# Optimization experiments

Measured on AMD Instinct MI355X. Metric: run time of the kernel, lower is better.

The kernel has to match this reference:

```python
import jax, jax.numpy as jnp
import numpy as np

B, L, D_MODEL = 4, 1024, 512
D_STATE, EXPAND, D_CONV = 16, 2, 4
D_INNER = EXPAND * D_MODEL
DT_RANK = D_MODEL // 16
NUM_LAYERS = 2
NL2 = 2 * NUM_LAYERS  # at/vt layer pairs, index 2*i -> at_i, 2*i+1 -> vt_i


def setup_inputs() -> dict:
    key = jax.random.key(0)
    ks = jax.random.split(key, 16)
    s = 0.02
    inp = {
        'a_x': jax.random.normal(ks[0], (B, L, D_MODEL), jnp.float32),
        'v_x': jax.random.normal(ks[1], (B, L, D_MODEL), jnp.float32),
        't_x': jax.random.normal(ks[2], (B, L, D_MODEL), jnp.float32),
        'in_proj_w': s * jax.random.normal(ks[3], (NL2, 2 * D_INNER, D_MODEL), jnp.float32),
        'conv_w': s * jax.random.normal(ks[4], (NL2, 2, D_INNER, D_CONV), jnp.float32),
        'conv_b': jnp.zeros((NL2, 2, D_INNER), jnp.float32),
        'xproj_w': s * jax.random.normal(ks[5], (NL2, 2, DT_RANK + 2 * D_STATE, D_INNER), jnp.float32),
        'dtproj_w': s * jax.random.normal(ks[6], (NL2, 2, D_INNER, DT_RANK), jnp.float32),
        'dtproj_b': 0.1 * jax.random.normal(ks[7], (NL2, 2, D_INNER), jnp.float32),
        'A_log': jnp.log(jnp.broadcast_to(jnp.arange(1.0, D_STATE + 1.0, dtype=jnp.float32), (NL2, 2, D_INNER, D_STATE))),
        'Dskip': jnp.ones((NL2, 2, D_INNER), jnp.float32),
        'out_proj_w': s * jax.random.normal(ks[8], (NL2, D_MODEL, D_INNER), jnp.float32),
        'ln_w': jnp.ones((NL2, 2, D_MODEL), jnp.float32),
        'ln_b': jnp.zeros((NL2, 2, D_MODEL), jnp.float32),
    }
    return inp


def layer_norm(x, w, b, eps=1e-6):
    m = jnp.mean(x, -1, keepdims=True)
    v = jnp.var(x, -1, keepdims=True)
    return (x - m) * jax.lax.rsqrt(v + eps) * w + b


def causal_conv1d(x, w, b):
    # x: (B,L,d), depthwise causal conv with kernel w: (d,k), bias b: (d,)
    y = jax.lax.conv_general_dilated(
        x.transpose(0, 2, 1), w[:, None, :], (1,), [(D_CONV - 1, 0)],
        feature_group_count=D_INNER,
        dimension_numbers=('NCH', 'OIH', 'NCH'))
    return y.transpose(0, 2, 1) + b


def selective_scan(u, dt, A, Bm, Cm, Dskip):
    # u,dt:(B,L,d)  A:(d,N)  Bm,Cm:(B,L,N)  Dskip:(d,)
    dA = jnp.exp(dt[..., None] * A)                    # (B,L,d,N)
    dBu = (dt * u)[..., None] * Bm[:, :, None, :]      # (B,L,d,N)

    def step(h, inp):
        dA_t, dBu_t, C_t = inp
        h = dA_t * h + dBu_t                           # (B,d,N)
        return h, jnp.einsum('bdn,bn->bd', h, C_t)

    h0 = jnp.zeros((u.shape[0], u.shape[2], D_STATE), u.dtype)
    xs = (jnp.moveaxis(dA, 1, 0), jnp.moveaxis(dBu, 1, 0), jnp.moveaxis(Cm, 1, 0))
    _, ys = jax.lax.scan(step, h0, xs)
    return jnp.moveaxis(ys, 0, 1) + u * Dskip


def _one_dir(x, cw, cb, xpw, dpw, dpb, A_log, Dskip):
    xc = jax.nn.silu(causal_conv1d(x, cw, cb))
    proj = xc @ xpw.T                                  # (B,L,dt_rank+2N)
    dt_r, Bm, Cm = jnp.split(proj, [DT_RANK, DT_RANK + D_STATE], axis=-1)
    dt = jax.nn.softplus(dt_r @ dpw.T + dpb)
    A = -jnp.exp(A_log)
    return selective_scan(xc, dt, A, Bm, Cm, Dskip)


def _bimamba(u, i, p):
    xz = u @ p['in_proj_w'][i].T
    x, z = jnp.split(xz, 2, axis=-1)
    yf = _one_dir(x, p['conv_w'][i, 0], p['conv_b'][i, 0], p['xproj_w'][i, 0],
                  p['dtproj_w'][i, 0], p['dtproj_b'][i, 0], p['A_log'][i, 0], p['Dskip'][i, 0])
    yb = _one_dir(x[:, ::-1], p['conv_w'][i, 1], p['conv_b'][i, 1], p['xproj_w'][i, 1],
                  p['dtproj_w'][i, 1], p['dtproj_b'][i, 1], p['A_log'][i, 1], p['Dskip'][i, 1])[:, ::-1]
    y = (yf + yb) * jax.nn.silu(z)
    return y @ p['out_proj_w'][i].T


def _enc_layer(a, t, i, p):
    ao = _bimamba(a, i, p)
    to = _bimamba(t, i, p)
    a_out = a + layer_norm(ao, p['ln_w'][i, 0], p['ln_b'][i, 0])
    t_out = t + layer_norm(to, p['ln_w'][i, 1], p['ln_b'][i, 1])
    return a_out, t_out


def reference(a_x, v_x, t_x, in_proj_w, conv_w, conv_b, xproj_w, dtproj_w, dtproj_b,
              A_log, Dskip, out_proj_w, ln_w, ln_b):
    p = dict(in_proj_w=in_proj_w, conv_w=conv_w, conv_b=conv_b, xproj_w=xproj_w,
             dtproj_w=dtproj_w, dtproj_b=dtproj_b, A_log=A_log, Dskip=Dskip,
             out_proj_w=out_proj_w, ln_w=ln_w, ln_b=ln_b)
    a_out, v_out, t_out = a_x, v_x, t_x
    for i in range(NUM_LAYERS):
        a_out, t_at = _enc_layer(a_out, t_out, 2 * i, p)
        v_out, t_vt = _enc_layer(v_out, t_out, 2 * i + 1, p)
        t_out = (t_at + t_vt) / 2
    return (a_out, v_out, t_out)
```

## Files before the change

### kernel.cpp

```cpp
#include <hip/hip_runtime.h>
#include <cstddef>

constexpr int B_      = 4;
constexpr int L_      = 1024;
constexpr int DM      = 512;
constexpr int DS      = 16;
constexpr int DI      = 1024;
constexpr int DTR     = 32;
constexpr int TOK     = B_ * L_;
constexpr int NLAYERS = 2;

constexpr size_t XZB = 0;
constexpr size_t XCB = (size_t)4 * TOK * 2 * DI * 2;
constexpr size_t PRB = XCB + (size_t)8 * TOK * DI * 2;
constexpr size_t WIB = PRB + (size_t)8 * TOK * 64 * 4;
constexpr size_t WOB = WIB + (size_t)4 * 2 * DI * DM * 2;
constexpr size_t WXB = WOB + (size_t)4 * DM * DI * 2;
constexpr size_t WS_NEED_BF = WXB + (size_t)8 * 64 * DI * 2;
constexpr size_t DTB2 = WS_NEED_BF;
constexpr size_t WS_NEED_DT = DTB2 + (size_t)8 * TOK * DI * 2;

constexpr int NCH = 16;
constexpr size_t PP_BYTE = (size_t)8 * 4 * NCH * 1024 * DS * 2;

#if defined(__has_builtin)
#if __has_builtin(__builtin_amdgcn_exp2f)
#define FAST_EXP2(x) __builtin_amdgcn_exp2f(x)
#endif
#endif
#ifndef FAST_EXP2
#define FAST_EXP2(x) exp2f(x)
#endif

__device__ __forceinline__ float silu_f(float x) { return x / (1.f + __expf(-x)); }

__device__ __forceinline__ float bf2f(unsigned short u) {
    union { unsigned u; float f; } v; v.u = ((unsigned)u) << 16; return v.f;
}
__device__ __forceinline__ unsigned short f2bf(float f) {
    union { float f; unsigned u; } v; v.f = f;
    unsigned r = v.u + 0x7FFFu + ((v.u >> 16) & 1u);
    return (unsigned short)(r >> 16);
}
__device__ __forceinline__ float softplus_f(float x) {
    float e = exp2f(-fabsf(x) * 1.44269504f);
    return fmaxf(x, 0.f) + 0.69314718f * log2f(1.f + e);
}

__device__ __forceinline__ size_t ovmap(size_t byte) {
    return ((byte >> 11) << 12) + (byte & 2047);
}
__device__ __forceinline__ void st4bf(char* b, size_t bank, size_t e, float4 v) {
    ushort4 o;
    o.x = f2bf(v.x); o.y = f2bf(v.y); o.z = f2bf(v.z); o.w = f2bf(v.w);
    *(ushort4*)(b + ovmap(bank + e * 2)) = o;
}
__device__ __forceinline__ float4 ld4bf(const char* b, size_t bank, size_t e) {
    ushort4 u = *(const ushort4*)(b + ovmap(bank + e * 2));
    return make_float4(bf2f(u.x), bf2f(u.y), bf2f(u.z), bf2f(u.w));
}

using bf16x8 = __attribute__((ext_vector_type(8))) short;
using f32x4v = __attribute__((ext_vector_type(4))) float;
using f32x2  = __attribute__((ext_vector_type(2))) float;

__device__ __forceinline__ void stage8(unsigned short* dst, const float* src) {
    float4 v0 = *(const float4*)src;
    float4 v1 = *(const float4*)(src + 4);
    ushort4 o0, o1;
    o0.x = f2bf(v0.x); o0.y = f2bf(v0.y); o0.z = f2bf(v0.z); o0.w = f2bf(v0.w);
    o1.x = f2bf(v1.x); o1.y = f2bf(v1.y); o1.z = f2bf(v1.z); o1.w = f2bf(v1.w);
    *(ushort4*)dst = o0;
    *(ushort4*)(dst + 4) = o1;
}
__device__ __forceinline__ void stage8(unsigned short* dst, const unsigned short* src) {
    *(uint4*)dst = *(const uint4*)src;
}

template<int N, int K, int LDKA, int BM, int BN, int FM, int FN, int EPI,
         typename TA, typename TW, typename TC>
__device__ __forceinline__ void mfma_gemm(const TA* __restrict__ A,
                                          const TW* __restrict__ W,
                                          TC* __restrict__ C,
                                          const float* __restrict__ bias)
{
    constexpr int WC  = BN / (FN * 16);
    constexpr int LDA = 40;
    __shared__ unsigned short As[BM * LDA];
    __shared__ unsigned short Bs[BN * LDA];
    const int tid  = threadIdx.x;
    const int lane = tid & 63, wid = tid >> 6;
    const int wr = wid / WC, wc = wid % WC;
    const int row0 = blockIdx.y * BM, col0 = blockIdx.x * BN;

    f32x4v acc[FM][FN] = {};
    constexpr int AITER = BM * 4 / 256;
    constexpr int BITER = BN * 4 / 256;

    for (int k0 = 0; k0 < K; k0 += 32) {
#pragma unroll
        for (int i = 0; i < AITER; ++i) {
            int f = i * 256 + tid;
            int row = f >> 2, c8 = (f & 3) * 8;
            stage8(&As[row * LDA + c8], A + (size_t)(row0 + row) * LDKA + k0 + c8);
        }
#pragma unroll
        for (int i = 0; i < BITER; ++i) {
            int f = i * 256 + tid;
            int row = f >> 2, c8 = (f & 3) * 8;
            stage8(&Bs[row * LDA + c8], W + (size_t)(col0 + row) * K + k0 + c8);
        }
        __syncthreads();
        bf16x8 af[FM], bfr[FN];
#pragma unroll
        for (int m = 0; m < FM; ++m)
            af[m] = *(const bf16x8*)&As[(wr * FM * 16 + m * 16 + (lane & 15)) * LDA + (lane >> 4) * 8];
#pragma unroll
        for (int n = 0; n < FN; ++n)
            bfr[n] = *(const bf16x8*)&Bs[(wc * FN * 16 + n * 16 + (lane & 15)) * LDA + (lane >> 4) * 8];
#pragma unroll
        for (int m = 0; m < FM; ++m)
#pragma unroll
            for (int n = 0; n < FN; ++n)
                acc[m][n] = __builtin_amdgcn_mfma_f32_16x16x32_bf16(af[m], bfr[n], acc[m][n], 0, 0, 0);
        __syncthreads();
    }
#pragma unroll
    for (int m = 0; m < FM; ++m) {
#pragma unroll
        for (int n = 0; n < FN; ++n) {
            int r0 = row0 + wr * FM * 16 + m * 16 + (lane >> 4) * 4;
            int c  = col0 + wc * FN * 16 + n * 16 + (lane & 15);
#pragma unroll
            for (int v = 0; v < 4; ++v) {
                float val = acc[m][n][v];
                if constexpr (EPI == 1) val = softplus_f(val + bias[c]);
                if constexpr (sizeof(TC) == 4)
                    C[(size_t)(r0 + v) * N + c] = val;
                else
                    C[(size_t)(r0 + v) * N + c] = f2bf(val);
            }
        }
    }
}

__global__ __launch_bounds__(256)
void k_wcast(const float* __restrict__ w1, const float* __restrict__ w2,
             const float* __restrict__ w3, unsigned short* __restrict__ o1,
             unsigned short* __restrict__ o2, unsigned short* __restrict__ o3)
{
    constexpr int N1 = 4 * 2 * DI * DM;
    constexpr int N2 = 4 * DM * DI;
    constexpr int N3 = 8 * 64 * DI;
    constexpr int T4 = (N1 + N2 + N3) / 4;
    for (int i = blockIdx.x * 256 + threadIdx.x; i < T4; i += gridDim.x * 256) {
        int e = i * 4;
        const float* src; unsigned short* dst; int off;
        if (e < N1)           { src = w1; dst = o1; off = e; }
        else if (e < N1 + N2) { src = w2; dst = o2; off = e - N1; }
        else                  { src = w3; dst = o3; off = e - N1 - N2; }
        float4 v = *(const float4*)(src + off);
        ushort4 o;
        o.x = f2bf(v.x); o.y = f2bf(v.y); o.z = f2bf(v.z); o.w = f2bf(v.w);
        *(ushort4*)(dst + off) = o;
    }
}

template<typename TW>
__global__ __launch_bounds__(256)
void k_inproj(const float* __restrict__ pa, const float* __restrict__ pt,
              const float* __restrict__ pv, const TW* __restrict__ w_all,
              unsigned short* __restrict__ xz, int layer)
{
    int g = blockIdx.z;
    const float* A = (g == 0) ? pa : (g == 2) ? pv : pt;
    int li = 2 * layer + (g >> 1);
    mfma_gemm<2 * DI, DM, DM, 128, 128, 4, 4, 0, float, TW, unsigned short>(
        A, w_all + (size_t)li * (2 * DI) * DM, xz + (size_t)g * TOK * (2 * DI), nullptr);
}

template<typename TW>
__global__ __launch_bounds__(256)
void k_xproj(const unsigned short* __restrict__ xc, const TW* __restrict__ xpw,
             float* __restrict__ proj, int layer)
{
    int gd = blockIdx.z;
    int dir = gd & 1;
    int li = 2 * layer + (gd >> 2);
    mfma_gemm<64, DI, DI, 128, 64, 4, 2, 0, unsigned short, TW, float>(
        xc + (size_t)gd * TOK * DI,
        xpw + (size_t)(li * 2 + dir) * 64 * DI,
        proj + (size_t)gd * TOK * 64, nullptr);
}

template<typename TW>
__global__ __launch_bounds__(256)
void k_outproj(const unsigned short* __restrict__ xcbuf, const TW* __restrict__ opw,
               float* __restrict__ yo, int layer)
{
    int g = blockIdx.z;
    int li = 2 * layer + (g >> 1);
    mfma_gemm<DM, DI, DI, 128, 128, 4, 4, 0, unsigned short, TW, float>(
        xcbuf + (size_t)(2 * g) * TOK * DI,
        opw + (size_t)li * DM * DI,
        yo + (size_t)g * TOK * DM, nullptr);
}

__global__ __launch_bounds__(256)
void k_dtmm(const float* __restrict__ proj, const float* __restrict__ dpw,
            const float* __restrict__ dpb, unsigned short* __restrict__ dt, int layer)
{
    int gd = blockIdx.z, dir = gd & 1;
    int li = 2 * layer + (gd >> 2);
    mfma_gemm<DI, 32, 64, 128, 128, 4, 4, 1, float, float, unsigned short>(
        proj + (size_t)gd * TOK * 64,
        dpw + (size_t)(li * 2 + dir) * DI * DTR,
        dt + (size_t)gd * TOK * DI,
        dpb + (size_t)(li * 2 + dir) * DI);
}

__global__ __launch_bounds__(256)
void k_conv(const unsigned short* __restrict__ xz, const float* __restrict__ cw,
            const float* __restrict__ cb, unsigned short* __restrict__ xc, int layer)
{
    constexpr int TT = 64;
    const int gd = blockIdx.y;
    const int g = gd >> 1, dir = gd & 1;
    const int li = 2 * layer + (g >> 1);
    const int d = threadIdx.x * 4;
    const int wbase = (li * 2 + dir) * DI + d;
    float w[4][4];
    *(float4*)w[0] = *(const float4*)(cw + (size_t)(wbase + 0) * 4);
    *(float4*)w[1] = *(const float4*)(cw + (size_t)(wbase + 1) * 4);
    *(float4*)w[2] = *(const float4*)(cw + (size_t)(wbase + 2) * 4);
    *(float4*)w[3] = *(const float4*)(cw + (size_t)(wbase + 3) * 4);
    const float4 bias = *(const float4*)(cb + wbase);

    const int t0 = blockIdx.x * TT;
    const int b = t0 >> 10, tt0 = t0 & 1023;
    const unsigned short* xcol = xz + ((size_t)g * TOK + (size_t)(b << 10)) * (2 * DI) + d;
    unsigned short* ocol = xc + ((size_t)gd * TOK + t0) * DI + d;

    auto ldx = [&](int tt, float* o) {
        if (tt >= 0 && tt < L_) {
            ushort4 v = *(const ushort4*)(xcol + (size_t)tt * (2 * DI));
            o[0] = bf2f(v.x); o[1] = bf2f(v.y); o[2] = bf2f(v.z); o[3] = bf2f(v.w);
        } else {
            o[0] = 0.f; o[1] = 0.f; o[2] = 0.f; o[3] = 0.f;
        }
    };

    if (dir == 0) {
        float x3[4], x2[4], x1[4], x0[4];
        ldx(tt0 - 3, x3); ldx(tt0 - 2, x2); ldx(tt0 - 1, x1);
#pragma unroll 4
        for (int j = 0; j < TT; ++j) {
            ldx(tt0 + j, x0);
            float r0 = bias.x + w[0][0] * x3[0] + w[0][1] * x2[0] + w[0][2] * x1[0] + w[0][3] * x0[0];
            float r1 = bias.y + w[1][0] * x3[1] + w[1][1] * x2[1] + w[1][2] * x1[1] + w[1][3] * x0[1];
            float r2 = bias.z + w[2][0] * x3[2] + w[2][1] * x2[2] + w[2][2] * x1[2] + w[2][3] * x0[2];
            float r3 = bias.w + w[3][0] * x3[3] + w[3][1] * x2[3] + w[3][2] * x1[3] + w[3][3] * x0[3];
            ushort4 o;
            o.x = f2bf(silu_f(r0)); o.y = f2bf(silu_f(r1));
            o.z = f2bf(silu_f(r2)); o.w = f2bf(silu_f(r3));
            *(ushort4*)(ocol + (size_t)j * DI) = o;
#pragma unroll
            for (int c = 0; c < 4; ++c) { x3[c] = x2[c]; x2[c] = x1[c]; x1[c] = x0[c]; }
        }
    } else {
        float p1[4], p2[4], p3[4], x0[4];
        ldx(tt0 + TT, p1); ldx(tt0 + TT + 1, p2); ldx(tt0 + TT + 2, p3);
#pragma unroll 4
        for (int j = TT - 1; j >= 0; --j) {
            ldx(tt0 + j, x0);
            float r0 = bias.x + w[0][3] * x0[0] + w[0][2] * p1[0] + w[0][1] * p2[0] + w[0][0] * p3[0];
            float r1 = bias.y + w[1][3] * x0[1] + w[1][2] * p1[1] + w[1][1] * p2[1] + w[1][0] * p3[1];
            float r2 = bias.z + w[2][3] * x0[2] + w[2][2] * p1[2] + w[2][1] * p2[2] + w[2][0] * p3[2];
            float r3 = bias.w + w[3][3] * x0[3] + w[3][2] * p1[3] + w[3][1] * p2[3] + w[3][0] * p3[3];
            ushort4 o;
            o.x = f2bf(silu_f(r0)); o.y = f2bf(silu_f(r1));
            o.z = f2bf(silu_f(r2)); o.w = f2bf(silu_f(r3));
            *(ushort4*)(ocol + (size_t)j * DI) = o;
#pragma unroll
            for (int c = 0; c < 4; ++c) { p3[c] = p2[c]; p2[c] = p1[c]; p1[c] = x0[c]; }
        }
    }
}

template<bool PW, bool P3, int DIR>
__device__ __forceinline__ void scan_core(
    unsigned short* __restrict__ xb, const unsigned short* __restrict__ db,
    const float* __restrict__ prb, unsigned short* __restrict__ us,
    unsigned short* __restrict__ ts,
    const int lane, const int q, f32x2 (&h2)[8], const float (&An2)[DS],
    const float a_base, float& cumdt, const float Dk)
{
    for (int sub = 0; sub < 4; ++sub) {
        const int s0 = q * 64 + sub * 16;
        const int tb0 = DIR ? (1008 - s0) : s0;
#pragma unroll
        for (int i = 0; i < 2; ++i) {
            int f = i * 64 + lane;
            int row = f >> 3, c8 = (f & 7) * 8;
            *(uint4*)&us[row * 64 + c8] = *(const uint4*)(xb + (size_t)(tb0 + row) * DI + c8);
            *(uint4*)&ts[row * 64 + c8] = *(const uint4*)(db + (size_t)(tb0 + row) * DI + c8);
        }
#pragma unroll
        for (int j = 0; j < 16; ++j) {
            const int row = DIR ? (15 - j) : j;
            const int t = tb0 + row;
            const float* prw = prb + (size_t)t * 64;
            float u   = bf2f(us[row * 64 + lane]);
            float dtv = bf2f(ts[row * 64 + lane]);
            float du = dtv * u;
            f32x2 du2 = {du, du};
            if constexpr (!P3) cumdt += dtv;
            f32x2 dA[8];
            if constexpr (PW) {
                float r  = FAST_EXP2(dtv * a_base);
                float r2 = r * r, r4 = r2 * r2, r8 = r4 * r4;
                f32x2 v2 = {r2, r2}, v4 = {r4, r4}, v8 = {r8, r8};
                dA[0] = f32x2{r, r2};
                dA[1] = dA[0] * v2;
                dA[2] = dA[0] * v4;
                dA[3] = dA[1] * v4;
                dA[4] = dA[0] * v8;
                dA[5] = dA[1] * v8;
                dA[6] = dA[2] * v8;
                dA[7] = dA[3] * v8;
            } else {
#pragma unroll
                for (int i2 = 0; i2 < 8; ++i2)
                    dA[i2] = f32x2{FAST_EXP2(dtv * An2[2 * i2]),
                                   FAST_EXP2(dtv * An2[2 * i2 + 1])};
            }
            f32x2 acc = {0.f, 0.f};
#pragma unroll
            for (int i2 = 0; i2 < 8; ++i2) {
                f32x2 Bv = *(const f32x2*)(prw + 32 + 2 * i2);
                h2[i2] = dA[i2] * h2[i2] + du2 * Bv;
                if constexpr (P3) {
                    f32x2 Cv = *(const f32x2*)(prw + 48 + 2 * i2);
                    acc += h2[i2] * Cv;
                }
            }
            if constexpr (P3)
                xb[(size_t)t * DI + lane] = f2bf(acc.x + acc.y + u * Dk);
        }
    }
}

template<bool PRE>
__global__ __launch_bounds__(256, 4)
void k_scan_p1(const unsigned short* __restrict__ xc, const float* __restrict__ proj,
               const unsigned short* __restrict__ dtb,
               const float* __restrict__ dpw, const float* __restrict__ dpb,
               const float* __restrict__ A_log, char* __restrict__ hsb, int layer)
{
    __shared__ unsigned short us[4][16 * 64];
    __shared__ unsigned short ts[PRE ? 4 : 1][PRE ? 16 * 64 : 1];
    const int tid = threadIdx.x, lane = tid & 63;
    const int wid = __builtin_amdgcn_readfirstlane(tid >> 6);
    const int chblk = blockIdx.x >> 2, qh = blockIdx.x & 3;
    const int q = qh * 4 + wid;
    const int b = blockIdx.y, gd = blockIdx.z;
    const int g = gd >> 1, dir = gd & 1;
    const int li = 2 * layer + (g >> 1);
    const int ch0 = chblk * 64;
    const int wl = (li * 2 + dir) * DI + ch0 + lane;

    float An2[DS];
    const float* Ap = A_log + (size_t)wl * DS;
#pragma unroll
    for (int n = 0; n < DS; ++n) An2[n] = -__expf(Ap[n]) * 1.44269504f;

    const unsigned short* xb = xc + ((size_t)gd * TOK + (size_t)b * L_) * DI + ch0;
    const unsigned short* db = dtb + ((size_t)gd * TOK + (size_t)b * L_) * DI + ch0;
    const float* prb = proj + ((size_t)gd * TOK + (size_t)b * L_) * 64;
    size_t e0 = ((((size_t)gd * 4 + b) * NCH + q) * 1024 + ch0 + lane) * DS;

    if constexpr (PRE) {
        const float a_base = An2[0];
        bool pwl = true;
#pragma unroll
        for (int n = 1; n < DS; ++n)
            pwl = pwl && (fabsf(An2[n] - (n + 1) * a_base) <= 1e-4f * fabsf(An2[n]));
        const bool pw = __all(pwl);
        f32x2 h2[8] = {};
        float cumdt = 0.f;
        unsigned short* xbm = (unsigned short*)xb;
        if (pw) {
            if (dir == 0)
                scan_core<true, false, 0>(xbm, db, prb, us[wid], ts[wid],
                                          lane, q, h2, An2, a_base, cumdt, 0.f);
            else
                scan_core<true, false, 1>(xbm, db, prb, us[wid], ts[wid],
                                          lane, q, h2, An2, a_base, cumdt, 0.f);
        } else {
            if (dir == 0)
                scan_core<false, false, 0>(xbm, db, prb, us[wid], ts[wid],
                                           lane, q, h2, An2, a_base, cumdt, 0.f);
            else
                scan_core<false, false, 1>(xbm, db, prb, us[wid], ts[wid],
                                           lane, q, h2, An2, a_base, cumdt, 0.f);
        }
        f32x2 pp[8];
        if (pw) {
            float R  = FAST_EXP2(cumdt * a_base);
            float R2 = R * R, R4 = R2 * R2, R8 = R4 * R4;
            f32x2 v2 = {R2, R2}, v4 = {R4, R4}, v8 = {R8, R8};
            pp[0] = f32x2{R, R2};
            pp[1] = pp[0] * v2; pp[2] = pp[0] * v4; pp[3] = pp[1] * v4;
            pp[4] = pp[0] * v8; pp[5] = pp[1] * v8; pp[6] = pp[2] * v8; pp[7] = pp[3] * v8;
        } else {
#pragma unroll
            for (int i2 = 0; i2 < 8; ++i2)
                pp[i2] = f32x2{FAST_EXP2(cumdt * An2[2 * i2]),
                               FAST_EXP2(cumdt * An2[2 * i2 + 1])};
        }
#pragma unroll
        for (int n = 0; n < DS; n += 4) {
            st4bf(hsb, 0, e0 + n, make_float4(h2[n / 2].x, h2[n / 2].y,
                                              h2[n / 2 + 1].x, h2[n / 2 + 1].y));
            st4bf(hsb, PP_BYTE, e0 + n, make_float4(pp[n / 2].x, pp[n / 2].y,
                                                    pp[n / 2 + 1].x, pp[n / 2 + 1].y));
        }
    } else {
        float w[DTR];
        const float* wp = dpw + (size_t)wl * DTR;
#pragma unroll
        for (int k = 0; k < DTR; ++k) w[k] = wp[k];
        const float bias = dpb[wl];
        float h[DS];
#pragma unroll
        for (int n = 0; n < DS; ++n) h[n] = 0.f;
        float cumdt = 0.f;
        for (int sub = 0; sub < 4; ++sub) {
            const int s0 = q * 64 + sub * 16;
            const int tb0 = dir ? (1008 - s0) : s0;
#pragma unroll
            for (int i = 0; i < 2; ++i) {
                int f = i * 64 + lane;
                int row = f >> 3, c8 = (f & 7) * 8;
                *(uint4*)&us[wid][row * 64 + c8] = *(const uint4*)(xb + (size_t)(tb0 + row) * DI + c8);
            }
            for (int j = 0; j < 16; ++j) {
                const int row = dir ? (15 - j) : j;
                const int t = tb0 + row;
                const float* prw = prb + (size_t)t * 64;
                float u = bf2f(us[wid][row * 64 + lane]);
                float a0 = bias;
#pragma unroll
                for (int k4 = 0; k4 < 8; ++k4) {
                    float4 p = *(const float4*)(prw + k4 * 4);
                    a0 += w[k4 * 4 + 0] * p.x + w[k4 * 4 + 1] * p.y
                        + w[k4 * 4 + 2] * p.z + w[k4 * 4 + 3] * p.w;
                }
                float dtv = softplus_f(a0);
                float du = dtv * u;
                cumdt += dtv;
#pragma unroll
                for (int n = 0; n < DS; ++n) {
                    float e = exp2f(dtv * An2[n]);
                    h[n] = e * h[n] + du * prw[32 + n];
                }
            }
        }
#pragma unroll
        for (int n = 0; n < DS; n += 4) {
            st4bf(hsb, 0, e0 + n, make_float4(h[n], h[n + 1], h[n + 2], h[n + 3]));
            float4 cp = make_float4(exp2f(cumdt * An2[n]),     exp2f(cumdt * An2[n + 1]),
                                    exp2f(cumdt * An2[n + 2]), exp2f(cumdt * An2[n + 3]));
            st4bf(hsb, PP_BYTE, e0 + n, cp);
        }
    }
}

__global__ __launch_bounds__(256)
void k_scan_p2(char* __restrict__ hsb)
{
    const int ch = blockIdx.x * 256 + threadIdx.x;
    const int b = blockIdx.y, gd = blockIdx.z;
    float h[DS];
#pragma unroll
    for (int n = 0; n < DS; ++n) h[n] = 0.f;
    for (int q = 0; q < NCH; ++q) {
        size_t e0 = ((((size_t)gd * 4 + b) * NCH + q) * 1024 + ch) * DS;
#pragma unroll
        for (int n = 0; n < DS; n += 4) {
            float4 hl = ld4bf(hsb, 0, e0 + n);
            float4 pp = ld4bf(hsb, PP_BYTE, e0 + n);
            st4bf(hsb, 0, e0 + n, make_float4(h[n], h[n + 1], h[n + 2], h[n + 3]));
            h[n + 0] = pp.x * h[n + 0] + hl.x;
            h[n + 1] = pp.y * h[n + 1] + hl.y;
            h[n + 2] = pp.z * h[n + 2] + hl.z;
            h[n + 3] = pp.w * h[n + 3] + hl.w;
        }
    }
}

template<bool PRE>
__global__ __launch_bounds__(256, 4)
void k_scan_p3(unsigned short* __restrict__ xc, const float* __restrict__ proj,
               const unsigned short* __restrict__ dtb,
               const float* __restrict__ dpw, const float* __restrict__ dpb,
               const float* __restrict__ A_log, const float* __restrict__ Dskip,
               const char* __restrict__ hsb, int layer)
{
    __shared__ unsigned short us[4][16 * 64];
    __shared__ unsigned short ts[PRE ? 4 : 1][PRE ? 16 * 64 : 1];
    const int tid = threadIdx.x, lane = tid & 63;
    const int wid = __builtin_amdgcn_readfirstlane(tid >> 6);
    const int chblk = blockIdx.x >> 2, qh = blockIdx.x & 3;
    const int q = qh * 4 + wid;
    const int b = blockIdx.y, gd = blockIdx.z;
    const int g = gd >> 1, dir = gd & 1;
    const int li = 2 * layer + (g >> 1);
    const int ch0 = chblk * 64;
    const int wl = (li * 2 + dir) * DI + ch0 + lane;

    float An2[DS];
    const float* Ap = A_log + (size_t)wl * DS;
#pragma unroll
    for (int n = 0; n < DS; ++n) An2[n] = -__expf(Ap[n]) * 1.44269504f;
    const float Dk = Dskip[wl];

    unsigned short* xb = xc + ((size_t)gd * TOK + (size_t)b * L_) * DI + ch0;
    const unsigned short* db = dtb + ((size_t)gd * TOK + (size_t)b * L_) * DI + ch0;
    const float* prb = proj + ((size_t)gd * TOK + (size_t)b * L_) * 64;
    size_t e0 = ((((size_t)gd * 4 + b) * NCH + q) * 1024 + ch0 + lane) * DS;

    if constexpr (PRE) {
        const float a_base = An2[0];
        bool pwl = true;
#pragma unroll
        for (int n = 1; n < DS; ++n)
            pwl = pwl && (fabsf(An2[n] - (n + 1) * a_base) <= 1e-4f * fabsf(An2[n]));
        const bool pw = __all(pwl);
        f32x2 h2[8];
#pragma unroll
        for (int n = 0; n < DS; n += 4) {
            float4 v = ld4bf(hsb, 0, e0 + n);
            h2[n / 2]     = f32x2{v.x, v.y};
            h2[n / 2 + 1] = f32x2{v.z, v.w};
        }
        float cumdt = 0.f;
        if (pw) {
            if (dir == 0)
                scan_core<true, true, 0>(xb, db, prb, us[wid], ts[wid],
                                         lane, q, h2, An2, a_base, cumdt, Dk);
            else
                scan_core<true, true, 1>(xb, db, prb, us[wid], ts[wid],
                                         lane, q, h2, An2, a_base, cumdt, Dk);
        } else {
            if (dir == 0)
                scan_core<false, true, 0>(xb, db, prb, us[wid], ts[wid],
                                          lane, q, h2, An2, a_base, cumdt, Dk);
            else
                scan_core<false, true, 1>(xb, db, prb, us[wid], ts[wid],
                                          lane, q, h2, An2, a_base, cumdt, Dk);
        }
    } else {
        float w[DTR];
        const float* wp = dpw + (size_t)wl * DTR;
#pragma unroll
        for (int k = 0; k < DTR; ++k) w[k] = wp[k];
        const float bias = dpb[wl];
        float h[DS];
#pragma unroll
        for (int n = 0; n < DS; n += 4) {
            float4 v = ld4bf(hsb, 0, e0 + n);
            h[n] = v.x; h[n + 1] = v.y; h[n + 2] = v.z; h[n + 3] = v.w;
        }
        for (int sub = 0; sub < 4; ++sub) {
            const int s0 = q * 64 + sub * 16;
            const int tb0 = dir ? (1008 - s0) : s0;
#pragma unroll
            for (int i = 0; i < 2; ++i) {
                int f = i * 64 + lane;
                int row = f >> 3, c8 = (f & 7) * 8;
                *(uint4*)&us[wid][row * 64 + c8] = *(const uint4*)(xb + (size_t)(tb0 + row) * DI + c8);
            }
            for (int j = 0; j < 16; ++j) {
                const int row = dir ? (15 - j) : j;
                const int t = tb0 + row;
                const float* prw = prb + (size_t)t * 64;
                float u = bf2f(us[wid][row * 64 + lane]);
                float a0 = bias;
#pragma unroll
                for (int k4 = 0; k4 < 8; ++k4) {
                    float4 p = *(const float4*)(prw + k4 * 4);
                    a0 += w[k4 * 4 + 0] * p.x + w[k4 * 4 + 1] * p.y
                        + w[k4 * 4 + 2] * p.z + w[k4 * 4 + 3] * p.w;
                }
                float dtv = softplus_f(a0);
                float du = dtv * u;
                float acc = 0.f;
#pragma unroll
                for (int n = 0; n < DS; ++n) {
                    float e = exp2f(dtv * An2[n]);
                    h[n] = e * h[n] + du * prw[32 + n];
                    acc += h[n] * prw[48 + n];
                }
                xb[(size_t)t * DI + lane] = f2bf(acc + u * Dk);
            }
        }
    }
}

__global__ __launch_bounds__(256)
void k_combine(unsigned short* __restrict__ xcbuf, const unsigned short* __restrict__ xz)
{
    int g = blockIdx.y;
    size_t idx = ((size_t)blockIdx.x * 256 + threadIdx.x) * 4;
    size_t m = idx >> 10, d = idx & 1023;
    unsigned short* yf_p = xcbuf + (size_t)(2 * g) * TOK * DI + idx;
    const unsigned short* yb_p = xcbuf + (size_t)(2 * g + 1) * TOK * DI + idx;
    const unsigned short* z_p  = xz + ((size_t)g * TOK + m) * (2 * DI) + DI + d;
    ushort4 yf = *(const ushort4*)yf_p;
    ushort4 yb = *(const ushort4*)yb_p;
    ushort4 zz = *(const ushort4*)z_p;
    ushort4 o;
    o.x = f2bf((bf2f(yf.x) + bf2f(yb.x)) * silu_f(bf2f(zz.x)));
    o.y = f2bf((bf2f(yf.y) + bf2f(yb.y)) * silu_f(bf2f(zz.y)));
    o.z = f2bf((bf2f(yf.z) + bf2f(yb.z)) * silu_f(bf2f(zz.z)));
    o.w = f2bf((bf2f(yf.w) + bf2f(yb.w)) * silu_f(bf2f(zz.w)));
    *(ushort4*)yf_p = o;
}

__device__ __forceinline__ void blk_red2(float& a, float& b, float* red)
{
#pragma unroll
    for (int o = 32; o; o >>= 1) {
        a += __shfl_down(a, o);
        b += __shfl_down(b, o);
    }
    int lane = threadIdx.x & 63, wid = threadIdx.x >> 6;
    if (lane == 0) { red[wid] = a; red[4 + wid] = b; }
    __syncthreads();
    a = red[0] + red[1] + red[2] + red[3];
    b = red[4] + red[5] + red[6] + red[7];
    __syncthreads();
}

__global__ __launch_bounds__(256)
void k_ln(const float* __restrict__ yo, const float* __restrict__ lnw,
          const float* __restrict__ lnb, const float* __restrict__ resA,
          const float* __restrict__ resT, const float* __restrict__ resV,
          float* __restrict__ outA, float* __restrict__ outT,
          float* __restrict__ outV, int layer)
{
    int tok = blockIdx.x, tid = threadIdx.x;
    __shared__ float red[8];
    float t1a = 0.f, t1b = 0.f;
#pragma unroll
    for (int s = 0; s < 4; ++s) {
        const float* p = yo + ((size_t)s * TOK + tok) * DM;
        float x0 = p[tid], x1 = p[tid + 256];
        float sm = x0 + x1, sq = x0 * x0 + x1 * x1;
        blk_red2(sm, sq, red);
        float mean = sm * (1.f / 512.f);
        float var  = sq * (1.f / 512.f) - mean * mean;
        float rstd = rsqrtf(var + 1e-6f);
        int li = 2 * layer + (s >> 1);
        int half = s & 1;
        const float* wv = lnw + (size_t)(li * 2 + half) * DM;
        const float* bv = lnb + (size_t)(li * 2 + half) * DM;
        float v0 = (x0 - mean) * rstd * wv[tid] + bv[tid];
        float v1 = (x1 - mean) * rstd * wv[tid + 256] + bv[tid + 256];
        size_t o0 = (size_t)tok * DM + tid, o1 = o0 + 256;
        if (s == 0) {
            outA[o0] = resA[o0] + v0;
            outA[o1] = resA[o1] + v1;
        } else if (s == 1) {
            t1a = v0; t1b = v1;
        } else if (s == 2) {
            outV[o0] = resV[o0] + v0;
            outV[o1] = resV[o1] + v1;
        } else {
            outT[o0] = resT[o0] + 0.5f * (t1a + v0);
            outT[o1] = resT[o1] + 0.5f * (t1b + v1);
        }
    }
}

extern "C" void kernel_launch(void* const* d_in, const int* in_sizes, int n_in,
                              void* d_out, int out_size, void* d_ws, size_t ws_size,
                              hipStream_t stream)
{
    (void)in_sizes; (void)n_in; (void)out_size;
    const float* a_x       = (const float*)d_in[0];
    const float* v_x       = (const float*)d_in[1];
    const float* t_x       = (const float*)d_in[2];
    const float* in_proj_w = (const float*)d_in[3];
    const float* conv_w    = (const float*)d_in[4];
    const float* conv_b    = (const float*)d_in[5];
    const float* xproj_w   = (const float*)d_in[6];
    const float* dtproj_w  = (const float*)d_in[7];
    const float* dtproj_b  = (const float*)d_in[8];
    const float* A_log     = (const float*)d_in[9];
    const float* Dskip     = (const float*)d_in[10];
    const float* out_proj_w= (const float*)d_in[11];
    const float* ln_w      = (const float*)d_in[12];
    const float* ln_b      = (const float*)d_in[13];

    char* wsb = (char*)d_ws;
    unsigned short* xz   = (unsigned short*)(wsb + XZB);
    unsigned short* xc   = (unsigned short*)(wsb + XCB);
    float*          proj = (float*)(wsb + PRB);
    float*          yo   = (float*)(wsb + XZB);
    char*           hsb  = wsb + XZB;
    unsigned short* wib  = (unsigned short*)(wsb + WIB);
    unsigned short* wob  = (unsigned short*)(wsb + WOB);
    unsigned short* wxb  = (unsigned short*)(wsb + WXB);
    unsigned short* dtb  = (unsigned short*)(wsb + DTB2);

    const bool wbf = (ws_size >= WS_NEED_BF);
    const bool pre = (ws_size >= WS_NEED_DT);

    float* out   = (float*)d_out;
    float* slotA = out;
    float* slotV = out + (size_t)TOK * DM;
    float* slotT = out + (size_t)2 * TOK * DM;

    if (wbf)
        k_wcast<<<dim3(1024), 256, 0, stream>>>(in_proj_w, out_proj_w, xproj_w,
                                                wib, wob, wxb);

    for (int layer = 0; layer < NLAYERS; ++layer) {
        const float* sa = layer ? slotA : a_x;
        const float* st = layer ? slotT : t_x;
        const float* sv = layer ? slotV : v_x;

        if (wbf)
            k_inproj<unsigned short><<<dim3(16, 32, 4), 256, 0, stream>>>(
                sa, st, sv, wib, xz, layer);
        else
            k_inproj<float><<<dim3(16, 32, 4), 256, 0, stream>>>(
                sa, st, sv, in_proj_w, xz, layer);

        k_conv<<<dim3(64, 8), 256, 0, stream>>>(xz, conv_w, conv_b, xc, layer);

        if (wbf)
            k_xproj<unsigned short><<<dim3(1, 32, 8), 256, 0, stream>>>(
                xc, wxb, proj, layer);
        else
            k_xproj<float><<<dim3(1, 32, 8), 256, 0, stream>>>(
                xc, xproj_w, proj, layer);

        if (pre) {
            k_dtmm<<<dim3(8, 32, 8), 256, 0, stream>>>(proj, dtproj_w, dtproj_b,
                                                       dtb, layer);
            k_scan_p1<true><<<dim3(64, 4, 8), 256, 0, stream>>>(
                xc, proj, dtb, dtproj_w, dtproj_b, A_log, hsb, layer);
            k_scan_p2<<<dim3(4, 4, 8), 256, 0, stream>>>(hsb);
            k_scan_p3<true><<<dim3(64, 4, 8), 256, 0, stream>>>(
                xc, proj, dtb, dtproj_w, dtproj_b, A_log, Dskip, hsb, layer);
        } else {
            k_scan_p1<false><<<dim3(64, 4, 8), 256, 0, stream>>>(
                xc, proj, dtb, dtproj_w, dtproj_b, A_log, hsb, layer);
            k_scan_p2<<<dim3(4, 4, 8), 256, 0, stream>>>(hsb);
            k_scan_p3<false><<<dim3(64, 4, 8), 256, 0, stream>>>(
                xc, proj, dtb, dtproj_w, dtproj_b, A_log, Dskip, hsb, layer);
        }

        k_combine<<<dim3(4096, 4), 256, 0, stream>>>(xc, xz);

        if (wbf)
            k_outproj<unsigned short><<<dim3(4, 32, 4), 256, 0, stream>>>(
                xc, wob, yo, layer);
        else
            k_outproj<float><<<dim3(4, 32, 4), 256, 0, stream>>>(
                xc, out_proj_w, yo, layer);

        k_ln<<<dim3(4096), 256, 0, stream>>>(yo, ln_w, ln_b, sa, st, sv,
                                             slotA, slotT, slotV, layer);
    }
}
```

Before: 732.8 us.

## Stage GEMM tiles with direct global-to-LDS loads and pre-cast activations to bf16

Adds a new GEMM path that moves A and W tiles straight from global memory into LDS with global_load_lds, skipping the register round trip. The in-projection, x-projection and out-projection GEMMs switch to this path. To supply bf16 input to the in-projection, a separate kernel first casts the fp32 layer inputs to bf16 in a new workspace buffer. This costs an extra launch and pass over the activations, and the new LDS layout has no padding, which may cause bank conflicts on the fragment reads.

After: 736.8 us. Within noise of the previous version (+0.5%).

```diff
diff --git a/kernel.cpp b/kernel.cpp
--- a/kernel.cpp
+++ b/kernel.cpp
@@ -19,6 +19,8 @@
 constexpr size_t WS_NEED_BF = WXB + (size_t)8 * 64 * DI * 2;
 constexpr size_t DTB2 = WS_NEED_BF;
 constexpr size_t WS_NEED_DT = DTB2 + (size_t)8 * TOK * DI * 2;
+constexpr size_t ACB  = WS_NEED_DT;
+constexpr size_t WS_NEED_AC = ACB + (size_t)3 * TOK * DM * 2;
 
 constexpr int NCH = 16;
 constexpr size_t PP_BYTE = (size_t)8 * 4 * NCH * 1024 * DS * 2;
@@ -64,6 +66,12 @@
 using f32x4v = __attribute__((ext_vector_type(4))) float;
 using f32x2  = __attribute__((ext_vector_type(2))) float;
 
+__device__ __forceinline__ void gld_lds16(const void* g, void* l) {
+    __builtin_amdgcn_global_load_lds(
+        (const __attribute__((address_space(1))) void*)g,
+        (__attribute__((address_space(3))) void*)l, 16, 0, 0);
+}
+
 __device__ __forceinline__ void stage8(unsigned short* dst, const float* src) {
     float4 v0 = *(const float4*)src;
     float4 v1 = *(const float4*)(src + 4);
@@ -139,6 +147,65 @@
                     C[(size_t)(r0 + v) * N + c] = val;
                 else
                     C[(size_t)(r0 + v) * N + c] = f2bf(val);
+            }
+        }
+    }
+}
+
+template<int N, int K, int LDKA, int BM, int BN, int FM, int FN, typename TC>
+__device__ __forceinline__ void mfma_gemm2(const unsigned short* __restrict__ A,
+                                           const unsigned short* __restrict__ W,
+                                           TC* __restrict__ C)
+{
+    constexpr int WC = BN / (FN * 16);
+    __shared__ unsigned short As[BM * 32];
+    __shared__ unsigned short Bs[BN * 32];
+    const int tid = threadIdx.x;
+    const int lane = tid & 63, wid = tid >> 6;
+    const int wr = wid / WC, wc = wid % WC;
+    const int row0 = blockIdx.y * BM, col0 = blockIdx.x * BN;
+    constexpr int SEGA = BM / 16, SEGB = BN / 16;
+    const int lrow = lane >> 2, lc8 = (lane & 3) * 8;
+
+    f32x4v acc[FM][FN] = {};
+    for (int k0 = 0; k0 < K; k0 += 32) {
+#pragma unroll
+        for (int c = 0; c < SEGA / 4; ++c) {
+            int s = wid * (SEGA / 4) + c;
+            gld_lds16(A + (size_t)(row0 + s * 16 + lrow) * LDKA + k0 + lc8, &As[s * 512]);
+        }
+#pragma unroll
+        for (int c = 0; c < SEGB / 4; ++c) {
+            int s = wid * (SEGB / 4) + c;
+            gld_lds16(W + (size_t)(col0 + s * 16 + lrow) * K + k0 + lc8, &Bs[s * 512]);
+        }
+        __syncthreads();
+        bf16x8 af[FM], bfr[FN];
+#pragma unroll
+        for (int m = 0; m < FM; ++m)
+            af[m] = *(const bf16x8*)&As[(wr * FM * 16 + m * 16 + (lane & 15)) * 32 + (lane >> 4) * 8];
+#pragma unroll
+        for (int n = 0; n < FN; ++n)
+            bfr[n] = *(const bf16x8*)&Bs[(wc * FN * 16 + n * 16 + (lane & 15)) * 32 + (lane >> 4) * 8];
+#pragma unroll
+        for (int m = 0; m < FM; ++m)
+#pragma unroll
+            for (int n = 0; n < FN; ++n)
+                acc[m][n] = __builtin_amdgcn_mfma_f32_16x16x32_bf16(af[m], bfr[n], acc[m][n], 0, 0, 0);
+        __syncthreads();
+    }
+#pragma unroll
+    for (int m = 0; m < FM; ++m) {
+#pragma unroll
+        for (int n = 0; n < FN; ++n) {
+            int r0 = row0 + wr * FM * 16 + m * 16 + (lane >> 4) * 4;
+            int c  = col0 + wc * FN * 16 + n * 16 + (lane & 15);
+#pragma unroll
+            for (int v = 0; v < 4; ++v) {
+                if constexpr (sizeof(TC) == 4)
+                    C[(size_t)(r0 + v) * N + c] = acc[m][n][v];
+                else
+                    C[(size_t)(r0 + v) * N + c] = f2bf(acc[m][n][v]);
             }
         }
     }
@@ -166,6 +233,20 @@
     }
 }
 
+__global__ __launch_bounds__(256)
+void k_acast(const float* __restrict__ pa, const float* __restrict__ pt,
+             const float* __restrict__ pv, unsigned short* __restrict__ ob)
+{
+    constexpr size_t NPER = (size_t)TOK * DM;
+    int w = blockIdx.y;
+    const float* s = (w == 0) ? pa : (w == 1) ? pt : pv;
+    size_t i = ((size_t)blockIdx.x * 256 + threadIdx.x) * 4;
+    float4 v = *(const float4*)(s + i);
+    ushort4 o;
+    o.x = f2bf(v.x); o.y = f2bf(v.y); o.z = f2bf(v.z); o.w = f2bf(v.w);
+    *(ushort4*)(ob + (size_t)w * NPER + i) = o;
+}
+
 template<typename TW>
 __global__ __launch_bounds__(256)
 void k_inproj(const float* __restrict__ pa, const float* __restrict__ pt,
@@ -177,6 +258,18 @@
     int li = 2 * layer + (g >> 1);
     mfma_gemm<2 * DI, DM, DM, 128, 128, 4, 4, 0, float, TW, unsigned short>(
         A, w_all + (size_t)li * (2 * DI) * DM, xz + (size_t)g * TOK * (2 * DI), nullptr);
+}
+
+__global__ __launch_bounds__(256)
+void k_inproj2(const unsigned short* __restrict__ ab, const unsigned short* __restrict__ wib,
+               unsigned short* __restrict__ xz, int layer)
+{
+    constexpr size_t NPER = (size_t)TOK * DM;
+    int g = blockIdx.z;
+    const unsigned short* A = ab + (size_t)((g == 0) ? 0 : (g == 2) ? 2 : 1) * NPER;
+    int li = 2 * layer + (g >> 1);
+    mfma_gemm2<2 * DI, DM, DM, 128, 128, 4, 4, unsigned short>(
+        A, wib + (size_t)li * (2 * DI) * DM, xz + (size_t)g * TOK * (2 * DI));
 }
 
 template<typename TW>
@@ -193,6 +286,19 @@
         proj + (size_t)gd * TOK * 64, nullptr);
 }
 
+__global__ __launch_bounds__(256)
+void k_xproj2(const unsigned short* __restrict__ xc, const unsigned short* __restrict__ xpw,
+              float* __restrict__ proj, int layer)
+{
+    int gd = blockIdx.z;
+    int dir = gd & 1;
+    int li = 2 * layer + (gd >> 2);
+    mfma_gemm2<64, DI, DI, 128, 64, 4, 2, float>(
+        xc + (size_t)gd * TOK * DI,
+        xpw + (size_t)(li * 2 + dir) * 64 * DI,
+        proj + (size_t)gd * TOK * 64);
+}
+
 template<typename TW>
 __global__ __launch_bounds__(256)
 void k_outproj(const unsigned short* __restrict__ xcbuf, const TW* __restrict__ opw,
@@ -204,6 +310,18 @@
         xcbuf + (size_t)(2 * g) * TOK * DI,
         opw + (size_t)li * DM * DI,
         yo + (size_t)g * TOK * DM, nullptr);
+}
+
+__global__ __launch_bounds__(256)
+void k_outproj2(const unsigned short* __restrict__ xcbuf, const unsigned short* __restrict__ opw,
+                float* __restrict__ yo, int layer)
+{
+    int g = blockIdx.z;
+    int li = 2 * layer + (g >> 1);
+    mfma_gemm2<DM, DI, DI, 128, 128, 4, 4, float>(
+        xcbuf + (size_t)(2 * g) * TOK * DI,
+        opw + (size_t)li * DM * DI,
+        yo + (size_t)g * TOK * DM);
 }
 
 __global__ __launch_bounds__(256)
@@ -714,9 +832,11 @@
     unsigned short* wob  = (unsigned short*)(wsb + WOB);
     unsigned short* wxb  = (unsigned short*)(wsb + WXB);
     unsigned short* dtb  = (unsigned short*)(wsb + DTB2);
+    unsigned short* abuf = (unsigned short*)(wsb + ACB);
 
     const bool wbf = (ws_size >= WS_NEED_BF);
     const bool pre = (ws_size >= WS_NEED_DT);
+    const bool ac  = (ws_size >= WS_NEED_AC) && wbf;
 
     float* out   = (float*)d_out;
     float* slotA = out;
@@ -732,16 +852,22 @@
         const float* st = layer ? slotT : t_x;
         const float* sv = layer ? slotV : v_x;
 
-        if (wbf)
+        if (ac) {
+            k_acast<<<dim3(2048, 3), 256, 0, stream>>>(sa, st, sv, abuf);
+            k_inproj2<<<dim3(16, 32, 4), 256, 0, stream>>>(abuf, wib, xz, layer);
+        } else if (wbf) {
             k_inproj<unsigned short><<<dim3(16, 32, 4), 256, 0, stream>>>(
                 sa, st, sv, wib, xz, layer);
-        else
+        } else {
             k_inproj<float><<<dim3(16, 32, 4), 256, 0, stream>>>(
                 sa, st, sv, in_proj_w, xz, layer);
+        }
 
         k_conv<<<dim3(64, 8), 256, 0, stream>>>(xz, conv_w, conv_b, xc, layer);
 
-        if (wbf)
+        if (ac)
+            k_xproj2<<<dim3(1, 32, 8), 256, 0, stream>>>(xc, wxb, proj, layer);
+        else if (wbf)
             k_xproj<unsigned short><<<dim3(1, 32, 8), 256, 0, stream>>>(
                 xc, wxb, proj, layer);
         else
@@ -766,7 +892,9 @@
 
         k_combine<<<dim3(4096, 4), 256, 0, stream>>>(xc, xz);
 
-        if (wbf)
+        if (ac)
+            k_outproj2<<<dim3(4, 32, 4), 256, 0, stream>>>(xc, wob, yo, layer);
+        else if (wbf)
             k_outproj<unsigned short><<<dim3(4, 32, 4), 256, 0, stream>>>(
                 xc, wob, yo, layer);
         else
```
